# Kernel tuning notes

Measured on AMD Instinct MI355X. Metric: run time of the kernel, lower is better.

The kernel has to match this reference:

```python
import jax, jax.numpy as jnp
import numpy as np
from jax.scipy.special import digamma, gammaln

NUM_CLASSES = 3
FOCAL_GAMMA = 2.0
LABEL_SMOOTHING = 0.1
EVIDENTIAL_W = 0.1
CONTRASTIVE_W = 0.1
BOUNDARY_W = 0.15
TRIPLET_W = 0.1
QUALITY_W = 0.1
TRIPLET_MARGIN = 1.5


def setup_inputs() -> dict:
    key = jax.random.key(0)
    k1, k2, k3 = jax.random.split(key, 3)
    B, D = 4096, 512
    logits = jax.random.normal(k1, (B, NUM_CLASSES), dtype=jnp.float32)
    targets = jax.random.randint(k2, (B,), 0, 3)
    features = jax.random.normal(k3, (B, D), dtype=jnp.float32)
    alpha = jax.random.uniform(jax.random.fold_in(key, 7), (B, NUM_CLASSES), dtype=jnp.float32)
    focal_alpha = jnp.array([1.0, 2.0, 1.5], dtype=jnp.float32)
    class_weights = jnp.array([1.0, 2.0, 1.5], dtype=jnp.float32)
    return {"logits": logits, "targets": targets, "features": features,
            "alpha": alpha, "epoch": 1, "focal_alpha": focal_alpha,
            "class_weights": class_weights}


def reference(logits, targets, features, alpha, epoch, focal_alpha, class_weights):
    B = logits.shape[0]
    C = NUM_CLASSES

    # ---- focal loss (label-smoothed CE, torch semantics) ----
    logp = jax.nn.log_softmax(logits, axis=1)                      # [B,C]
    nll = -jnp.take_along_axis(logp, targets[:, None], axis=1)[:, 0]
    ce_ls = (1.0 - LABEL_SMOOTHING) * nll + LABEL_SMOOTHING * (-logp.mean(axis=1))
    pt = jnp.exp(-ce_ls)
    focal = (focal_alpha[targets] * (1.0 - pt) ** FOCAL_GAMMA * ce_ls).mean()

    # ---- weighted CE (torch weighted mean: sum(w*nll)/sum(w)) ----
    w = class_weights[targets]
    ce = (w * nll).sum() / w.sum()

    # ---- enhanced boundary loss ----
    probs = jax.nn.softmax(logits, axis=1)
    real = targets == 0
    semi = targets == 1
    syn = targets == 2
    rb = jnp.where(real, probs[:, 1] + 0.6 * probs[:, 2], 0.0).sum()
    sb = jnp.where(syn, probs[:, 1] + 0.4 * probs[:, 0], 0.0).sum()
    mb = jnp.where(semi, 1.0 - probs[:, 1] + 0.3 * (probs[:, 0] + probs[:, 2]), 0.0).sum()
    boundary = (rb + sb + 4.5 * mb) / (B + 1e-8)

    total = 0.4 * focal + 0.3 * ce + BOUNDARY_W * boundary

    # ---- normalized features and pairwise cosine-sim matrix ----
    norms = jnp.linalg.norm(features, axis=1, keepdims=True)
    f = features / jnp.maximum(norms, 1e-12)
    sim = f @ f.T                                                  # [B,B]
    same = targets[:, None] == targets[None, :]
    eye = jnp.eye(B, dtype=bool)

    # ---- enhanced contrastive loss ----
    pos = jnp.where(same, (1.0 - sim) ** 2, 0.0).sum()
    neg = jnp.where(~same, jnp.clip(sim - 0.2, 0.0) ** 2, 0.0).sum()
    semi_pair = semi[:, None] & semi[None, :]
    semi_l = jnp.where(semi_pair, (1.0 - sim) ** 2, 0.0).sum()
    contrastive = (pos + neg + 4.0 * semi_l) / (B * B + 1e-8)

    # ---- enhanced triplet loss (batch-hard, vectorized) ----
    d2 = jnp.clip(2.0 - 2.0 * sim, 0.0)
    dist = jnp.sqrt(jnp.where(eye, 1.0, d2))  # diag masked; safe sqrt
    pos_mask = same & ~eye
    neg_mask = ~same
    hp = jnp.max(jnp.where(pos_mask, dist, -jnp.inf), axis=1)
    hn = jnp.min(jnp.where(neg_mask, dist, jnp.inf), axis=1)
    valid = pos_mask.any(axis=1) & neg_mask.any(axis=1)
    margin = TRIPLET_MARGIN * jnp.where(targets == 1, 2.5, 1.0)
    tl = jax.nn.relu(hp - hn + margin)
    cnt = valid.sum()
    triplet = jnp.where(cnt > 0,
                        jnp.where(valid, tl, 0.0).sum() / jnp.maximum(cnt, 1),
                        0.0)

    # ---- quality-invariant loss (upper-tri same-class pairs) ----
    upper = jnp.triu(jnp.ones((B, B), dtype=bool), k=1)
    qmask = same & upper
    npairs = qmask.sum()
    q = jnp.where(qmask, (1.0 - sim) ** 2, 0.0).sum() / jnp.maximum(npairs, 1)
    frac2 = syn.astype(jnp.float32).mean()
    q = q * jnp.where(syn.sum() > 0, 1.0 + 2.5 * frac2, 1.0)
    quality = jnp.where(npairs > 0, q, 0.0)

    # ---- evidential loss ----
    onehot = jax.nn.one_hot(targets, C, dtype=jnp.float32)
    S = alpha.sum(axis=1, keepdims=True) + 1e-8
    likelihood = (onehot * (digamma(S) - digamma(alpha + 1e-8))).sum(axis=1)
    at = onehot + (1.0 - onehot) * alpha
    ats = at.sum(axis=1) + 1e-8
    kl = (gammaln(ats) - gammaln(at + 1e-8).sum(axis=1)
          + ((at - 1.0) * (digamma(at + 1e-8) - digamma(ats[:, None] + 1e-8))).sum(axis=1))
    annealing = min(1.0, (epoch / 25.0) ** 2)
    evidential = likelihood.mean() + annealing * 0.2 * kl.mean()

    total = (total + CONTRASTIVE_W * contrastive + TRIPLET_W * triplet
             + QUALITY_W * quality + EVIDENTIAL_W * evidential)
    return total
```

## Files before the change

### kernel.cpp

```cpp
#include <hip/hip_runtime.h>
#include <hip/hip_bf16.h>
#include <cstdint>

typedef __attribute__((ext_vector_type(8))) __bf16 bf8;
typedef __attribute__((ext_vector_type(4))) float f32x4;

__device__ __forceinline__ unsigned mapf(float x){
  unsigned u = __float_as_uint(x);
  return (u & 0x80000000u) ? ~u : (u | 0x80000000u);
}
__device__ __forceinline__ float unmapf(unsigned u){
  return __uint_as_float((u & 0x80000000u) ? (u & 0x7FFFFFFFu) : ~u);
}

__device__ float digammaf_(float x){
  float r = 0.f;
  while (x < 6.f){ r -= 1.f/x; x += 1.f; }
  float inv = 1.f/x, inv2 = inv*inv;
  r += logf(x) - 0.5f*inv
     - inv2*(0.08333333333f - inv2*(0.008333333333f - inv2*0.003968253968f));
  return r;
}

__global__ __launch_bounds__(256) void k_prep(const float* __restrict__ feat,
    __bf16* __restrict__ fb2,
    const float* __restrict__ logits, const int* __restrict__ targets,
    const float* __restrict__ alpha,  const float* __restrict__ fa,
    const float* __restrict__ cw, int B, int D,
    float* __restrict__ psum, unsigned* rowMinU, unsigned* rowMaxU){
  int bid = blockIdx.x, tid = threadIdx.x;
  int wave = tid >> 6, lane = tid & 63;

  int row = bid*4 + wave;
  const float* src = feat + (size_t)row*D;
  float ss = 0.f;
  for (int c = lane*4; c < D; c += 64*4){
    float4 v = *(const float4*)(src + c);
    ss += v.x*v.x + v.y*v.y + v.z*v.z + v.w*v.w;
  }
  #pragma unroll
  for (int off=32; off; off>>=1) ss += __shfl_xor(ss, off);
  float inv = 1.f / fmaxf(sqrtf(ss), 1e-12f);

  int p = row >> 6, r = row & 63;
  int mi = r >> 4, l16r = r & 15;
  int NCH = D >> 5;
  for (int c = lane*8; c < D; c += 64*8){
    float4 v0 = *(const float4*)(src + c);
    float4 v1 = *(const float4*)(src + c + 4);
    bf8 o;
    o[0]=(__bf16)(v0.x*inv); o[1]=(__bf16)(v0.y*inv);
    o[2]=(__bf16)(v0.z*inv); o[3]=(__bf16)(v0.w*inv);
    o[4]=(__bf16)(v1.x*inv); o[5]=(__bf16)(v1.y*inv);
    o[6]=(__bf16)(v1.z*inv); o[7]=(__bf16)(v1.w*inv);
    int cc = c >> 5;
    int q  = (c >> 3) & 3;
    size_t off = ((size_t)(p*NCH + cc)*4 + mi)*512 + (q*16 + l16r)*8;
    *(bf8*)(fb2 + off) = o;
  }

  if (tid < 4){ rowMinU[bid*4+tid] = 0xFFFFFFFFu; rowMaxU[bid*4+tid] = 0u; }

  if (wave == 0){
    float r0=0.f,r1=0.f,r2=0.f,r3=0.f,r4=0.f,r5=0.f;
    if (lane < 4){
      int i = bid*4 + lane;
      float l0=logits[3*i], l1=logits[3*i+1], l2=logits[3*i+2];
      int t = targets[i];
      float m = fmaxf(l0, fmaxf(l1,l2));
      float e0=expf(l0-m), e1=expf(l1-m), e2=expf(l2-m);
      float se = e0+e1+e2;
      float lse = m + logf(se);
      float lp0=l0-lse, lp1=l1-lse, lp2=l2-lse;
      float lpt = (t==0)?lp0:((t==1)?lp1:lp2);
      float nll = -lpt;
      float ce_ls = 0.9f*nll + 0.1f*(-(lp0+lp1+lp2)*(1.f/3.f));
      float pt = expf(-ce_ls);
      float om = 1.f - pt;
      float focal_i = fa[t]*om*om*ce_ls;
      float w = cw[t];
      float ce_n = w*nll, ce_d = w;
      float p0=e0/se, p1=e1/se, p2=e2/se;
      float bnd;
      if (t==0)      bnd = p1 + 0.6f*p2;
      else if (t==2) bnd = p1 + 0.4f*p0;
      else           bnd = 4.5f*(1.f - p1 + 0.3f*(p0+p2));
      float a0=alpha[3*i], a1=alpha[3*i+1], a2=alpha[3*i+2];
      float S = a0+a1+a2 + 1e-8f;
      float at_ = (t==0)?a0:((t==1)?a1:a2);
      float lik = digammaf_(S) - digammaf_(at_ + 1e-8f);
      float b0 = (t==0)?1.f:a0, b1 = (t==1)?1.f:a1, b2 = (t==2)?1.f:a2;
      float ats = b0+b1+b2 + 1e-8f;
      float psa = digammaf_(ats + 1e-8f);
      float kl = lgammaf(ats)
         - (lgammaf(b0+1e-8f)+lgammaf(b1+1e-8f)+lgammaf(b2+1e-8f))
         + (b0-1.f)*(digammaf_(b0+1e-8f)-psa)
         + (b1-1.f)*(digammaf_(b1+1e-8f)-psa)
         + (b2-1.f)*(digammaf_(b2+1e-8f)-psa);
      r0=focal_i; r1=ce_n; r2=ce_d; r3=bnd; r4=lik; r5=kl;
    }
    float s0 = ((__shfl(r0,0)+__shfl(r0,1))+__shfl(r0,2))+__shfl(r0,3);
    float s1 = ((__shfl(r1,0)+__shfl(r1,1))+__shfl(r1,2))+__shfl(r1,3);
    float s2 = ((__shfl(r2,0)+__shfl(r2,1))+__shfl(r2,2))+__shfl(r2,3);
    float s3 = ((__shfl(r3,0)+__shfl(r3,1))+__shfl(r3,2))+__shfl(r3,3);
    float s4 = ((__shfl(r4,0)+__shfl(r4,1))+__shfl(r4,2))+__shfl(r4,3);
    float s5 = ((__shfl(r5,0)+__shfl(r5,1))+__shfl(r5,2))+__shfl(r5,3);
    if (lane == 0){
      psum[bid*8+0]=s0; psum[bid*8+1]=s1; psum[bid*8+2]=s2;
      psum[bid*8+3]=s3; psum[bid*8+4]=s4; psum[bid*8+5]=s5;
    }
  }
}

__global__ __launch_bounds__(64) void k_pairs(const __bf16* __restrict__ fb2,
    const int* __restrict__ targets, int B, int D,
    float* __restrict__ pairPart, unsigned* rowMinU, unsigned* rowMaxU){
  int t = blockIdx.x;
  int bx = (int)((sqrtf(8.f*(float)t + 1.f) - 1.f)*0.5f);
  while ((bx+1)*(bx+2)/2 <= t) bx++;
  while (bx*(bx+1)/2 > t) bx--;
  int by = t - bx*(bx+1)/2;
  bool isDiag = (by == bx);
  int rowBase = by*32, colBase = bx*32;

  int lane = threadIdx.x;
  int quad = lane >> 4, l16 = lane & 15;
  int NCH = D >> 5;

  const __bf16* pA = fb2 + ((size_t)(by>>1)*NCH*4 + (by&1)*2)*512 + lane*8;
  const __bf16* pB = fb2 + ((size_t)(bx>>1)*NCH*4 + (bx&1)*2)*512 + lane*8;

  f32x4 C[2][2] = {};
  bf8 A0[2], B0[2], A1[2], B1[2];

  #define LOADF(AD, BD, it) do{ \
    AD[0] = *(const bf8*)(pA + (size_t)(it)*2048);        \
    AD[1] = *(const bf8*)(pA + (size_t)(it)*2048 + 512);  \
    BD[0] = *(const bf8*)(pB + (size_t)(it)*2048);        \
    BD[1] = *(const bf8*)(pB + (size_t)(it)*2048 + 512);  \
  }while(0)

  #define COMPUTE(AF, BF) do{ \
    _Pragma("unroll") \
    for (int mi=0; mi<2; mi++) \
      _Pragma("unroll") \
      for (int ni=0; ni<2; ni++) \
        C[mi][ni] = __builtin_amdgcn_mfma_f32_16x16x32_bf16(AF[mi], BF[ni], C[mi][ni], 0,0,0); \
  }while(0)

  LOADF(A0, B0, 0);
  for (int it=0; it<NCH; it+=2){
    LOADF(A1, B1, it+1);
    COMPUTE(A0, B0);
    if (it+2 < NCH) LOADF(A0, B0, it+2);
    COMPUTE(A1, B1);
  }
  #undef LOADF
  #undef COMPUTE

  int tcol[2];
  #pragma unroll
  for (int ni=0; ni<2; ni++) tcol[ni] = targets[colBase + ni*16 + l16];

  float pos=0.f, neg=0.f, semi=0.f, diag=0.f;
  float cmin[2], cmax[2];
  #pragma unroll
  for (int ni=0; ni<2; ni++){ cmin[ni]=2.f; cmax[ni]=-2.f; }

  #pragma unroll
  for (int mi=0; mi<2; mi++){
    #pragma unroll
    for (int r=0; r<4; r++){
      int rl = mi*16 + quad*4 + r;
      int row = rowBase + rl;
      int tr = targets[row];
      float vmin = 2.f, vmax = -2.f;
      #pragma unroll
      for (int ni=0; ni<2; ni++){
        int col = colBase + ni*16 + l16;
        float s = C[mi][ni][r];
        if (tr == tcol[ni]){
          float omv = 1.f - s;
          float q = omv*omv;
          pos += q;
          if (tr == 1) semi += q;
          if (row == col) diag += q;
          else {
            vmin = fminf(vmin, s);
            cmin[ni] = fminf(cmin[ni], s);
          }
        } else {
          float c0 = fmaxf(s - 0.2f, 0.f);
          neg += c0*c0;
          vmax = fmaxf(vmax, s);
          cmax[ni] = fmaxf(cmax[ni], s);
        }
      }
      #pragma unroll
      for (int off=1; off<16; off<<=1){
        vmin = fminf(vmin, __shfl_xor(vmin, off));
        vmax = fmaxf(vmax, __shfl_xor(vmax, off));
      }
      if (l16 == 0){
        atomicMin(&rowMinU[row], mapf(vmin));
        atomicMax(&rowMaxU[row], mapf(vmax));
      }
    }
  }

  if (!isDiag){
    #pragma unroll
    for (int ni=0; ni<2; ni++){
      float cn = cmin[ni], cx = cmax[ni];
      cn = fminf(cn, __shfl_xor(cn, 16)); cn = fminf(cn, __shfl_xor(cn, 32));
      cx = fmaxf(cx, __shfl_xor(cx, 16)); cx = fmaxf(cx, __shfl_xor(cx, 32));
      if (quad == 0){
        int col = colBase + ni*16 + l16;
        atomicMin(&rowMinU[col], mapf(cn));
        atomicMax(&rowMaxU[col], mapf(cx));
      }
    }
  }

  #pragma unroll
  for (int off=32; off; off>>=1){
    pos  += __shfl_xor(pos, off);
    neg  += __shfl_xor(neg, off);
    semi += __shfl_xor(semi, off);
    diag += __shfl_xor(diag, off);
  }
  if (lane == 0){
    float fac = isDiag ? 1.f : 2.f;
    pairPart[blockIdx.x*4+0] = pos*fac;
    pairPart[blockIdx.x*4+1] = neg*fac;
    pairPart[blockIdx.x*4+2] = semi*fac;
    pairPart[blockIdx.x*4+3] = diag;
  }
}

__global__ __launch_bounds__(1024) void k_final(const int* __restrict__ targets,
    const int* __restrict__ epoch_p, int B, int nprep, int nblk,
    const float* __restrict__ pairPart, const float* __restrict__ psum,
    const unsigned* rowMinU, const unsigned* rowMaxU, float* out){
  int tid = threadIdx.x, wave = tid>>6, lane = tid&63;
  __shared__ float redf[16][8];
  __shared__ int   redi[16][4];
  __shared__ float tot6[6];
  __shared__ int   cns[3];
  __shared__ float ptot[4];

  {
    int c0=0,c1=0,c2=0;
    for (int i4 = tid; i4 < B/4; i4 += 1024){
      int4 tv = ((const int4*)targets)[i4];
      c0 += (tv.x==0)+(tv.y==0)+(tv.z==0)+(tv.w==0);
      c1 += (tv.x==1)+(tv.y==1)+(tv.z==1)+(tv.w==1);
      c2 += (tv.x==2)+(tv.y==2)+(tv.z==2)+(tv.w==2);
    }
    #pragma unroll
    for (int off=32; off; off>>=1){
      c0+=__shfl_xor(c0,off); c1+=__shfl_xor(c1,off); c2+=__shfl_xor(c2,off);
    }
    if (lane==0){ redi[wave][0]=c0; redi[wave][1]=c1; redi[wave][2]=c2; }
  }
  {
    float v0=0,v1=0,v2=0,v3=0,v4=0,v5=0;
    for (int s = tid; s < nprep; s += 1024){
      float4 a = *(const float4*)(psum + s*8);
      float4 b = *(const float4*)(psum + s*8 + 4);
      v0+=a.x; v1+=a.y; v2+=a.z; v3+=a.w; v4+=b.x; v5+=b.y;
    }
    #pragma unroll
    for (int off=32; off; off>>=1){
      v0+=__shfl_xor(v0,off); v1+=__shfl_xor(v1,off); v2+=__shfl_xor(v2,off);
      v3+=__shfl_xor(v3,off); v4+=__shfl_xor(v4,off); v5+=__shfl_xor(v5,off);
    }
    if (lane==0){
      redf[wave][0]=v0; redf[wave][1]=v1; redf[wave][2]=v2;
      redf[wave][3]=v3; redf[wave][4]=v4; redf[wave][5]=v5;
    }
  }
  __syncthreads();
  if (tid == 0){
    int c0=0,c1=0,c2=0;
    float v[6]={0,0,0,0,0,0};
    for (int w2=0; w2<16; w2++){
      c0+=redi[w2][0]; c1+=redi[w2][1]; c2+=redi[w2][2];
      for (int j=0;j<6;j++) v[j]+=redf[w2][j];
    }
    cns[0]=c0; cns[1]=c1; cns[2]=c2;
    for (int j=0;j<6;j++) tot6[j]=v[j];
  }
  __syncthreads();

  {
    float p=0,n=0,s2=0,d=0;
    for (int s = tid; s < nblk; s += 1024){
      float4 a = *(const float4*)(pairPart + s*4);
      p+=a.x; n+=a.y; s2+=a.z; d+=a.w;
    }
    #pragma unroll
    for (int off=32; off; off>>=1){
      p+=__shfl_xor(p,off); n+=__shfl_xor(n,off);
      s2+=__shfl_xor(s2,off); d+=__shfl_xor(d,off);
    }
    if (lane==0){ redf[wave][0]=p; redf[wave][1]=n; redf[wave][2]=s2; redf[wave][3]=d; }
  }
  __syncthreads();
  if (tid == 0){
    float a=0,b=0,c=0,e=0;
    for (int w2=0; w2<16; w2++){ a+=redf[w2][0]; b+=redf[w2][1]; c+=redf[w2][2]; e+=redf[w2][3]; }
    ptot[0]=a; ptot[1]=b; ptot[2]=c; ptot[3]=e;
  }
  __syncthreads();

  int n0=cns[0], n1=cns[1], n2=cns[2];

  float tsum = 0.f, tcnt = 0.f;
  for (int i = tid; i < B; i += 1024){
    int t = targets[i];
    int nt = (t==0)?n0:((t==1)?n1:n2);
    if (nt - 1 > 0 && B - nt > 0){
      float mn = unmapf(rowMinU[i]);
      float mx = unmapf(rowMaxU[i]);
      float hp = sqrtf(fmaxf(2.f - 2.f*mn, 0.f));
      float hn = sqrtf(fmaxf(2.f - 2.f*mx, 0.f));
      float margin = 1.5f * ((t==1) ? 2.5f : 1.f);
      float tl = fmaxf(hp - hn + margin, 0.f);
      tsum += tl; tcnt += 1.f;
    }
  }
  #pragma unroll
  for (int off=32; off; off>>=1){ tsum += __shfl_xor(tsum, off); tcnt += __shfl_xor(tcnt, off); }
  if (lane==0){ redf[wave][6]=tsum; redf[wave][7]=tcnt; }
  __syncthreads();

  if (tid==0){
    float ts=0, tn=0;
    for (int w2=0; w2<16; w2++){ ts+=redf[w2][6]; tn+=redf[w2][7]; }
    float triplet = (tn > 0.f) ? ts / fmaxf(tn, 1.f) : 0.f;
    float pos=ptot[0], neg=ptot[1], semi=ptot[2], diag=ptot[3];
    float Bf = (float)B;
    float focal = tot6[0] / Bf;
    float ce = tot6[1] / tot6[2];
    float boundary = tot6[3] / (Bf + 1e-8f);
    float contrastive = (pos + neg + 4.f*semi) / (Bf*Bf + 1e-8f);
    long long npl = ((long long)n0*(n0-1) + (long long)n1*(n1-1) + (long long)n2*(n2-1))/2;
    float qsum = (pos - diag) * 0.5f;
    float q = qsum / (float)(npl > 0 ? npl : 1);
    if (n2 > 0) q *= (1.f + 2.5f * ((float)n2 / Bf));
    float quality = (npl > 0) ? q : 0.f;
    int ep = epoch_p[0];
    float er = (float)ep / 25.f;
    float ann = fminf(1.f, er*er);
    float evidential = tot6[4]/Bf + ann*0.2f*tot6[5]/Bf;
    float total = 0.4f*focal + 0.3f*ce + 0.15f*boundary
                + 0.1f*contrastive + 0.1f*triplet + 0.1f*quality + 0.1f*evidential;
    out[0] = total;
  }
}

extern "C" void kernel_launch(void* const* d_in, const int* in_sizes, int n_in,
                              void* d_out, int out_size, void* d_ws, size_t ws_size,
                              hipStream_t stream){
  const float* logits   = (const float*)d_in[0];
  const int*   targets  = (const int*)d_in[1];
  const float* features = (const float*)d_in[2];
  const float* alpha    = (const float*)d_in[3];
  const int*   epoch    = (const int*)d_in[4];
  const float* fa       = (const float*)d_in[5];
  const float* cw       = (const float*)d_in[6];
  int B = in_sizes[1];
  int D = in_sizes[2] / B;
  int nprep = B/4;
  int T  = B / 32;
  int nblk = T*(T+1)/2;

  char* ws = (char*)d_ws;
  float*    psum     = (float*)(ws);
  float*    pairPart = (float*)(ws + 65536);
  unsigned* rowMinU  = (unsigned*)(ws + 65536 + 196608);
  unsigned* rowMaxU  = (unsigned*)(ws + 65536 + 196608 + (size_t)B*4);
  __bf16*   fb2      = (__bf16*)(ws + 65536 + 196608 + (size_t)B*8);

  k_prep <<<nprep, 256, 0, stream>>>(features, fb2, logits, targets, alpha, fa, cw,
                                     B, D, psum, rowMinU, rowMaxU);
  k_pairs<<<nblk, 64, 0, stream>>>(fb2, targets, B, D, pairPart, rowMinU, rowMaxU);
  k_final<<<1, 1024, 0, stream>>>(targets, epoch, B, nprep, nblk, pairPart, psum,
                                  rowMinU, rowMaxU, (float*)d_out);
}
```

Measured before the change: 128.9 us.

## Compute two column tiles per block sharing row-tile loads in pairwise sim kernel

```diff
diff --git a/kernel.cpp b/kernel.cpp
--- a/kernel.cpp
+++ b/kernel.cpp
@@ -112,115 +112,155 @@
   }
 }
 
-__global__ __launch_bounds__(64) void k_pairs(const __bf16* __restrict__ fb2,
+__global__ __launch_bounds__(64, 4) void k_pairs(const __bf16* __restrict__ fb2,
     const int* __restrict__ targets, int B, int D,
     float* __restrict__ pairPart, unsigned* rowMinU, unsigned* rowMaxU){
-  int t = blockIdx.x;
-  int bx = (int)((sqrtf(8.f*(float)t + 1.f) - 1.f)*0.5f);
-  while ((bx+1)*(bx+2)/2 <= t) bx++;
-  while (bx*(bx+1)/2 > t) bx--;
-  int by = t - bx*(bx+1)/2;
-  bool isDiag = (by == bx);
-  int rowBase = by*32, colBase = bx*32;
-
+  int NBY = B >> 5;
+  int bid = blockIdx.x;
+  int by  = bid % NBY;
+  int p   = bid / NBY;
+  int bx0 = by + 2*p;
   int lane = threadIdx.x;
+  if (bx0 >= NBY){
+    if (lane == 0) *(float4*)(pairPart + bid*4) = make_float4(0.f,0.f,0.f,0.f);
+    return;
+  }
+  int bx1 = bx0 + 1;
+  bool hasT1 = (bx1 < NBY);
+  bool isDiag0 = (bx0 == by);
+  int rowBase = by*32, colBase0 = bx0*32, colBase1 = bx1*32;
+
   int quad = lane >> 4, l16 = lane & 15;
   int NCH = D >> 5;
 
-  const __bf16* pA = fb2 + ((size_t)(by>>1)*NCH*4 + (by&1)*2)*512 + lane*8;
-  const __bf16* pB = fb2 + ((size_t)(bx>>1)*NCH*4 + (bx&1)*2)*512 + lane*8;
-
-  f32x4 C[2][2] = {};
-  bf8 A0[2], B0[2], A1[2], B1[2];
-
-  #define LOADF(AD, BD, it) do{ \
-    AD[0] = *(const bf8*)(pA + (size_t)(it)*2048);        \
-    AD[1] = *(const bf8*)(pA + (size_t)(it)*2048 + 512);  \
-    BD[0] = *(const bf8*)(pB + (size_t)(it)*2048);        \
-    BD[1] = *(const bf8*)(pB + (size_t)(it)*2048 + 512);  \
+  const __bf16* pA  = fb2 + ((size_t)(by >>1)*NCH*4 + (by &1)*2)*512 + lane*8;
+  const __bf16* pB0 = fb2 + ((size_t)(bx0>>1)*NCH*4 + (bx0&1)*2)*512 + lane*8;
+  const __bf16* pB1 = hasT1
+      ? fb2 + ((size_t)(bx1>>1)*NCH*4 + (bx1&1)*2)*512 + lane*8
+      : pB0;
+
+  f32x4 C0[2][2] = {};
+  f32x4 C1[2][2] = {};
+  bf8 As0[2], Bs00[2], Bs10[2];
+  bf8 As1[2], Bs01[2], Bs11[2];
+
+  #define LOADS(As, B0s, B1s, it) do{ \
+    As[0]  = *(const bf8*)(pA  + (size_t)(it)*2048); \
+    As[1]  = *(const bf8*)(pA  + (size_t)(it)*2048 + 512); \
+    B0s[0] = *(const bf8*)(pB0 + (size_t)(it)*2048); \
+    B0s[1] = *(const bf8*)(pB0 + (size_t)(it)*2048 + 512); \
+    B1s[0] = *(const bf8*)(pB1 + (size_t)(it)*2048); \
+    B1s[1] = *(const bf8*)(pB1 + (size_t)(it)*2048 + 512); \
   }while(0)
 
-  #define COMPUTE(AF, BF) do{ \
+  #define COMP(As, B0s, B1s) do{ \
     _Pragma("unroll") \
     for (int mi=0; mi<2; mi++) \
       _Pragma("unroll") \
       for (int ni=0; ni<2; ni++) \
-        C[mi][ni] = __builtin_amdgcn_mfma_f32_16x16x32_bf16(AF[mi], BF[ni], C[mi][ni], 0,0,0); \
+        C0[mi][ni] = __builtin_amdgcn_mfma_f32_16x16x32_bf16(As[mi], B0s[ni], C0[mi][ni], 0,0,0); \
+    _Pragma("unroll") \
+    for (int mi=0; mi<2; mi++) \
+      _Pragma("unroll") \
+      for (int ni=0; ni<2; ni++) \
+        C1[mi][ni] = __builtin_amdgcn_mfma_f32_16x16x32_bf16(As[mi], B1s[ni], C1[mi][ni], 0,0,0); \
   }while(0)
 
-  LOADF(A0, B0, 0);
+  LOADS(As0, Bs00, Bs10, 0);
   for (int it=0; it<NCH; it+=2){
-    LOADF(A1, B1, it+1);
-    COMPUTE(A0, B0);
-    if (it+2 < NCH) LOADF(A0, B0, it+2);
-    COMPUTE(A1, B1);
-  }
-  #undef LOADF
-  #undef COMPUTE
-
-  int tcol[2];
-  #pragma unroll
-  for (int ni=0; ni<2; ni++) tcol[ni] = targets[colBase + ni*16 + l16];
-
-  float pos=0.f, neg=0.f, semi=0.f, diag=0.f;
-  float cmin[2], cmax[2];
-  #pragma unroll
-  for (int ni=0; ni<2; ni++){ cmin[ni]=2.f; cmax[ni]=-2.f; }
-
-  #pragma unroll
-  for (int mi=0; mi<2; mi++){
+    LOADS(As1, Bs01, Bs11, it+1);
+    COMP(As0, Bs00, Bs10);
+    if (it+2 < NCH) LOADS(As0, Bs00, Bs10, it+2);
+    COMP(As1, Bs01, Bs11);
+  }
+  #undef LOADS
+  #undef COMP
+
+  int trow = targets[rowBase + (lane & 31)];
+  int tcol0[2], tcol1[2];
+  tcol0[0] = targets[colBase0 + l16];
+  tcol0[1] = targets[colBase0 + 16 + l16];
+  tcol1[0] = hasT1 ? targets[colBase1 + l16]      : 0;
+  tcol1[1] = hasT1 ? targets[colBase1 + 16 + l16] : 0;
+
+  float rowMinReg = 2.f, rowMaxReg = -2.f;
+  float posA=0.f, negA=0.f, semiA=0.f, diagA=0.f;
+  float posB=0.f, negB=0.f, semiB=0.f, diagB=0.f;
+
+  auto epi = [&](const f32x4 (&Cx)[2][2], const int (&tcolx)[2], int colBasex,
+                 bool isD, float& posx, float& negx, float& semix, float& diagx){
+    float cmin[2] = {2.f, 2.f}, cmax[2] = {-2.f, -2.f};
     #pragma unroll
-    for (int r=0; r<4; r++){
-      int rl = mi*16 + quad*4 + r;
-      int row = rowBase + rl;
-      int tr = targets[row];
-      float vmin = 2.f, vmax = -2.f;
+    for (int mi=0; mi<2; mi++){
+      #pragma unroll
+      for (int r=0; r<4; r++){
+        int rl = mi*16 + quad*4 + r;
+        int row = rowBase + rl;
+        int tr = __shfl(trow, rl);
+        float vmin = 2.f, vmax = -2.f;
+        #pragma unroll
+        for (int ni=0; ni<2; ni++){
+          int col = colBasex + ni*16 + l16;
+          float s = Cx[mi][ni][r];
+          if (tr == tcolx[ni]){
+            float omv = 1.f - s;
+            float q = omv*omv;
+            posx += q;
+            if (tr == 1) semix += q;
+            if (row == col) diagx += q;
+            else {
+              vmin = fminf(vmin, s);
+              cmin[ni] = fminf(cmin[ni], s);
+            }
+          } else {
+            float c0 = fmaxf(s - 0.2f, 0.f);
+            negx += c0*c0;
+            vmax = fmaxf(vmax, s);
+            cmax[ni] = fmaxf(cmax[ni], s);
+          }
+        }
+        #pragma unroll
+        for (int off=1; off<16; off<<=1){
+          vmin = fminf(vmin, __shfl_xor(vmin, off));
+          vmax = fmaxf(vmax, __shfl_xor(vmax, off));
+        }
+        if (l16 == mi*4 + r){
+          rowMinReg = fminf(rowMinReg, vmin);
+          rowMaxReg = fmaxf(rowMaxReg, vmax);
+        }
+      }
+    }
+    if (!isD){
       #pragma unroll
       for (int ni=0; ni<2; ni++){
-        int col = colBase + ni*16 + l16;
-        float s = C[mi][ni][r];
-        if (tr == tcol[ni]){
-          float omv = 1.f - s;
-          float q = omv*omv;
-          pos += q;
-          if (tr == 1) semi += q;
-          if (row == col) diag += q;
-          else {
-            vmin = fminf(vmin, s);
-            cmin[ni] = fminf(cmin[ni], s);
-          }
-        } else {
-          float c0 = fmaxf(s - 0.2f, 0.f);
-          neg += c0*c0;
-          vmax = fmaxf(vmax, s);
-          cmax[ni] = fmaxf(cmax[ni], s);
-        }
+        cmin[ni] = fminf(cmin[ni], __shfl_xor(cmin[ni], 16));
+        cmin[ni] = fminf(cmin[ni], __shfl_xor(cmin[ni], 32));
+        cmax[ni] = fmaxf(cmax[ni], __shfl_xor(cmax[ni], 16));
+        cmax[ni] = fmaxf(cmax[ni], __shfl_xor(cmax[ni], 32));
       }
-      #pragma unroll
-      for (int off=1; off<16; off<<=1){
-        vmin = fminf(vmin, __shfl_xor(vmin, off));
-        vmax = fmaxf(vmax, __shfl_xor(vmax, off));
+      if (lane < 32){
+        float cnv = (lane < 16) ? cmin[0] : cmin[1];
+        float cxv = (lane < 16) ? cmax[0] : cmax[1];
+        atomicMin(&rowMinU[colBasex + lane], mapf(cnv));
+        atomicMax(&rowMaxU[colBasex + lane], mapf(cxv));
       }
-      if (l16 == 0){
-        atomicMin(&rowMinU[row], mapf(vmin));
-        atomicMax(&rowMaxU[row], mapf(vmax));
-      }
-    }
-  }
-
-  if (!isDiag){
-    #pragma unroll
-    for (int ni=0; ni<2; ni++){
-      float cn = cmin[ni], cx = cmax[ni];
-      cn = fminf(cn, __shfl_xor(cn, 16)); cn = fminf(cn, __shfl_xor(cn, 32));
-      cx = fmaxf(cx, __shfl_xor(cx, 16)); cx = fmaxf(cx, __shfl_xor(cx, 32));
-      if (quad == 0){
-        int col = colBase + ni*16 + l16;
-        atomicMin(&rowMinU[col], mapf(cn));
-        atomicMax(&rowMaxU[col], mapf(cx));
-      }
-    }
-  }
+    }
+  };
+
+  epi(C0, tcol0, colBase0, isDiag0, posA, negA, semiA, diagA);
+  if (hasT1) epi(C1, tcol1, colBase1, false, posB, negB, semiB, diagB);
+
+  if (l16 < 8){
+    int row = rowBase + quad*4 + (l16 & 3) + 16*(l16 >> 2);
+    atomicMin(&rowMinU[row], mapf(rowMinReg));
+    atomicMax(&rowMaxU[row], mapf(rowMaxReg));
+  }
+
+  float fac0 = isDiag0 ? 1.f : 2.f;
+  float pos  = posA*fac0 + posB*2.f;
+  float neg  = negA*fac0 + negB*2.f;
+  float semi = semiA*fac0 + semiB*2.f;
+  float diag = diagA;
 
   #pragma unroll
   for (int off=32; off; off>>=1){
@@ -229,13 +269,8 @@
     semi += __shfl_xor(semi, off);
     diag += __shfl_xor(diag, off);
   }
-  if (lane == 0){
-    float fac = isDiag ? 1.f : 2.f;
-    pairPart[blockIdx.x*4+0] = pos*fac;
-    pairPart[blockIdx.x*4+1] = neg*fac;
-    pairPart[blockIdx.x*4+2] = semi*fac;
-    pairPart[blockIdx.x*4+3] = diag;
-  }
+  if (lane == 0)
+    *(float4*)(pairPart + bid*4) = make_float4(pos, neg, semi, diag);
 }
 
 __global__ __launch_bounds__(1024) void k_final(const int* __restrict__ targets,
@@ -373,8 +408,9 @@
   int B = in_sizes[1];
   int D = in_sizes[2] / B;
   int nprep = B/4;
-  int T  = B / 32;
-  int nblk = T*(T+1)/2;
+  int NBY = B / 32;
+  int PMAX = (NBY + 1) / 2;
+  int nblk = NBY * PMAX;
 
   char* ws = (char*)d_ws;
   float*    psum     = (float*)(ws);
```

Measured after the change: 122.7 us. 1.05x faster.
